# Optimization experiments

Measured on AMD Instinct MI355X. Metric: run time of the kernel, lower is better.

Reference implementation:

```python
import jax, jax.numpy as jnp
import numpy as np


def setup_inputs() -> dict:
    key = jax.random.key(0)
    k1, k2, k3 = jax.random.split(key, 3)
    N = 16384
    y = jax.random.normal(k1, (N,), dtype=jnp.float32)
    y_hat = jax.random.normal(k2, (N,), dtype=jnp.float32)
    status = jax.random.randint(k3, (N,), 0, 2, dtype=jnp.int32)
    return {"y": y, "y_hat": y_hat, "status": status}


def reference(y, y_hat, status):
    # Pairwise concordance index over all pairs i < j.
    # ge[i, j] = y[i] >= y[j]; le[i, j] = y[i] <= y[j]
    N = y.shape[0]
    ge = y[:, None] >= y[None, :]
    le = y[:, None] <= y[None, :]
    ge_hat = y_hat[:, None] >= y_hat[None, :]
    le_hat = y_hat[:, None] <= y_hat[None, :]
    st_i = (status == 1)[:, None]  # astatus_1 broadcast over j
    st_j = (status == 1)[None, :]  # bstatus_1 broadcast over i
    # upper-triangular mask (strict): pairs with j > i
    mask = jnp.triu(jnp.ones((N, N), dtype=bool), k=1)

    c1 = ge & ge_hat & st_j
    c2 = le & le_hat & st_i
    cc = (c1 | c2) & mask

    tp1 = le & st_i
    tp2 = ge & st_j
    tp = (tp1 | tp2) & mask

    c = jnp.sum(cc.astype(jnp.int32)).astype(jnp.float32)
    total_pairs = jnp.sum(tp.astype(jnp.int32)).astype(jnp.float32)
    return c / total_pairs
```

## Files before the change

kernel.cpp:

```cpp
#include <hip/hip_runtime.h>


#define BLOCK 256
#define TJ 256
#define IT 4
#define TI (BLOCK * IT)
#define GRID_PAIRS 1024


__global__ __launch_bounds__(256) void compact_kernel(
    const float* __restrict__ y, const float* __restrict__ yh,
    const int* __restrict__ status, int n,
    unsigned* __restrict__ cnts,
    float2* __restrict__ p1, float2* __restrict__ p0)
{
    int i = blockIdx.x * 256 + threadIdx.x;
    int lane = threadIdx.x & 63;
    bool act = i < n;
    float yv  = act ? y[i]  : 0.0f;
    float yhv = act ? yh[i] : 0.0f;
    bool st = act && (status[i] == 1);
    unsigned long long m1 = __ballot(st);
    unsigned long long m0 = __ballot(act && !st);
    unsigned long long lt = (1ull << lane) - 1ull;
    unsigned b1 = 0, b0 = 0;
    if (lane == 0) {
        b1 = atomicAdd(&cnts[0], (unsigned)__popcll(m1));
        b0 = atomicAdd(&cnts[1], (unsigned)__popcll(m0));
    }
    b1 = __shfl(b1, 0, 64);
    b0 = __shfl(b0, 0, 64);
    if (st) {
        p1[b1 + (unsigned)__popcll(m1 & lt)] = make_float2(yv, yhv);
    } else if (act) {
        p0[b0 + (unsigned)__popcll(m0 & lt)] = make_float2(yv, yhv);
    }
}

__global__ __launch_bounds__(BLOCK) void pairs_kernel(
    const unsigned* __restrict__ cnts,
    const float2* __restrict__ p1, const float2* __restrict__ p0,
    unsigned long long* __restrict__ acc, unsigned* __restrict__ done,
    float* __restrict__ out)
{
    __shared__ float2 s_j[TJ];
    const int tid = threadIdx.x;
    const unsigned K = cnts[0], M = cnts[1];
    const int ntJ  = (int)((K + TJ - 1) / TJ);
    const int ntIA = (int)((K + TI - 1) / TI);
    const int ntIB = (int)((M + TI - 1) / TI);
    const int ntA  = ntIA * ntJ;
    const int ntot = ntA + ntIB * ntJ;
    const float PINF = __int_as_float(0x7f800000);
    const float NINF = __int_as_float(0xff800000);

    unsigned accNE = 0, accBC = 0, accBG = 0;

    for (int t = blockIdx.x; t < ntot; t += gridDim.x) {
        bool isA = t < ntA;
        int tt = isA ? t : t - ntA;
        int ti = tt / ntJ;
        int tj = tt - ti * ntJ;

        {
            int jidx = tj * TJ + tid;
            float2 jv = p1[jidx];
            if ((unsigned)jidx >= K) jv = make_float2(PINF, NINF);
            s_j[tid] = jv;
        }
        __syncthreads();

        const float2* pi = isA ? p1 : p0;
        unsigned ilim = isA ? K : M;
        float2 v0, v1, v2, v3;
        {
            int ib = ti * TI + tid;
            float2 sA = make_float2(NINF, PINF);
            float2 sB = make_float2(NINF, NINF);
            float2 sent = isA ? sA : sB;
            v0 = pi[ib];              if ((unsigned)(ib)             >= ilim) v0 = sent;
            v1 = pi[ib + BLOCK];      if ((unsigned)(ib + BLOCK)     >= ilim) v1 = sent;
            v2 = pi[ib + 2 * BLOCK];  if ((unsigned)(ib + 2 * BLOCK) >= ilim) v2 = sent;
            v3 = pi[ib + 3 * BLOCK];  if ((unsigned)(ib + 3 * BLOCK) >= ilim) v3 = sent;
        }

        if (isA) {
            unsigned n0 = 0, n1 = 0;
#pragma unroll 8
            for (int jj = 0; jj < TJ; ++jj) {
                float2 p = s_j[jj];
                n0 += (unsigned)((v0.x >= p.x) != (v0.y >= p.y));
                n1 += (unsigned)((v1.x >= p.x) != (v1.y >= p.y));
                n0 += (unsigned)((v2.x >= p.x) != (v2.y >= p.y));
                n1 += (unsigned)((v3.x >= p.x) != (v3.y >= p.y));
            }
            accNE += n0 + n1;
        } else {
            unsigned g0 = 0, g1 = 0, c0 = 0, c1 = 0;
#pragma unroll 8
            for (int jj = 0; jj < TJ; ++jj) {
                float2 p = s_j[jj];
                bool a0 = v0.x >= p.x, b0 = v0.y >= p.y;
                bool a1 = v1.x >= p.x, b1 = v1.y >= p.y;
                bool a2 = v2.x >= p.x, b2 = v2.y >= p.y;
                bool a3 = v3.x >= p.x, b3 = v3.y >= p.y;
                g0 += (unsigned)a0; c0 += (unsigned)(a0 & b0);
                g1 += (unsigned)a1; c1 += (unsigned)(a1 & b1);
                g0 += (unsigned)a2; c0 += (unsigned)(a2 & b2);
                g1 += (unsigned)a3; c1 += (unsigned)(a3 & b3);
            }
            accBG += g0 + g1; accBC += c0 + c1;
        }
        __syncthreads();
    }

#pragma unroll
    for (int off = 32; off > 0; off >>= 1) {
        accNE += __shfl_down(accNE, off, 64);
        accBC += __shfl_down(accBC, off, 64);
        accBG += __shfl_down(accBG, off, 64);
    }
    __shared__ unsigned rN[4], rC[4], rG[4];
    int wav = tid >> 6, lane = tid & 63;
    if (lane == 0) { rN[wav] = accNE; rC[wav] = accBC; rG[wav] = accBG; }
    __syncthreads();
    if (tid == 0) {
        unsigned long long ne = (unsigned long long)rN[0] + rN[1] + rN[2] + rN[3];
        unsigned long long bc = (unsigned long long)rC[0] + rC[1] + rC[2] + rC[3];
        unsigned long long bg = (unsigned long long)rG[0] + rG[1] + rG[2] + rG[3];
        if (ne) atomicAdd(&acc[0], ne);
        if (bc) atomicAdd(&acc[1], bc);
        if (bg) atomicAdd(&acc[2], bg);
        __threadfence();
        if (atomicAdd(done, 1u) == (unsigned)(gridDim.x - 1)) {
            __threadfence();
            unsigned long long NE = atomicAdd(&acc[0], 0ull);
            unsigned long long BC = atomicAdd(&acc[1], 0ull);
            unsigned long long BG = atomicAdd(&acc[2], 0ull);
            unsigned long long Kl = K;
            unsigned long long slots = (unsigned long long)(ntIA * TI) *
                                       (unsigned long long)(ntJ * TJ);
            unsigned long long EQ = slots - NE;
            unsigned long long CC = EQ + 2ull * BC;
            unsigned long long TP = Kl * Kl + 2ull * BG;
            long long cn = (long long)CC - (long long)Kl;
            long long tn = (long long)TP - (long long)Kl;
            out[0] = (float)cn / (float)tn;
        }
    }
}

extern "C" void kernel_launch(void* const* d_in, const int* in_sizes, int n_in,
                              void* d_out, int out_size, void* d_ws, size_t ws_size,
                              hipStream_t stream) {
    const float* y      = (const float*)d_in[0];
    const float* y_hat  = (const float*)d_in[1];
    const int*   status = (const int*)d_in[2];
    float* out = (float*)d_out;
    int n = in_sizes[0];
    int stride = n + 1024;

    char* base = (char*)d_ws;
    unsigned* cnts = (unsigned*)base;
    unsigned long long* acc = (unsigned long long*)(base + 8);
    unsigned* done = (unsigned*)(base + 32);
    float2* p1 = (float2*)(base + 64);
    float2* p0 = p1 + stride;

    hipMemsetAsync(base, 0, 64, stream);

    hipLaunchKernelGGL(compact_kernel, dim3((n + 255) / 256), dim3(256), 0, stream,
                       y, y_hat, status, n, cnts, p1, p0);

    hipLaunchKernelGGL(pairs_kernel, dim3(GRID_PAIRS), dim3(BLOCK), 0, stream,
                       cnts, p1, p0, acc, done, out);
}
```

Measured before the change: 97.75 us.

## Use dynamic atomic tile scheduling with smaller i-tiles and NaN-select compare trick

Replaces the static grid-stride tile loop with a global atomic tile counter, so blocks pull work dynamically and load stays balanced. The i-tile is halved (2 items per thread instead of 4), which doubles the tile count and shared-memory loads per comparison but gives finer scheduling granularity. The concordant count now uses a select-to-NaN followed by one compare in place of an AND of two compares. This adds one atomic and one barrier per tile.

```diff
diff --git a/kernel.cpp b/kernel.cpp
--- a/kernel.cpp
+++ b/kernel.cpp
@@ -3,7 +3,7 @@
 
 #define BLOCK 256
 #define TJ 256
-#define IT 4
+#define IT 2
 #define TI (BLOCK * IT)
 #define GRID_PAIRS 1024
 
@@ -41,9 +41,10 @@
     const unsigned* __restrict__ cnts,
     const float2* __restrict__ p1, const float2* __restrict__ p0,
     unsigned long long* __restrict__ acc, unsigned* __restrict__ done,
-    float* __restrict__ out)
+    unsigned* __restrict__ tile_ctr, float* __restrict__ out)
 {
     __shared__ float2 s_j[TJ];
+    __shared__ int s_tile;
     const int tid = threadIdx.x;
     const unsigned K = cnts[0], M = cnts[1];
     const int ntJ  = (int)((K + TJ - 1) / TJ);
@@ -53,10 +54,16 @@
     const int ntot = ntA + ntIB * ntJ;
     const float PINF = __int_as_float(0x7f800000);
     const float NINF = __int_as_float(0xff800000);
+    const float NANF = __int_as_float(0x7fc00000);
 
-    unsigned accNE = 0, accBC = 0, accBG = 0;
+    unsigned aNE0 = 0, aNE1 = 0, aBG0 = 0, aBG1 = 0, aBC0 = 0, aBC1 = 0;
 
-    for (int t = blockIdx.x; t < ntot; t += gridDim.x) {
+    for (;;) {
+        if (tid == 0) s_tile = (int)atomicAdd(tile_ctr, 1u);
+        __syncthreads();
+        int t = s_tile;
+        if (t >= ntot) break;
+
         bool isA = t < ntA;
         int tt = isA ? t : t - ntA;
         int ti = tt / ntJ;
@@ -72,17 +79,12 @@
 
         const float2* pi = isA ? p1 : p0;
         unsigned ilim = isA ? K : M;
-        float2 v0, v1, v2, v3;
-        {
-            int ib = ti * TI + tid;
-            float2 sA = make_float2(NINF, PINF);
-            float2 sB = make_float2(NINF, NINF);
-            float2 sent = isA ? sA : sB;
-            v0 = pi[ib];              if ((unsigned)(ib)             >= ilim) v0 = sent;
-            v1 = pi[ib + BLOCK];      if ((unsigned)(ib + BLOCK)     >= ilim) v1 = sent;
-            v2 = pi[ib + 2 * BLOCK];  if ((unsigned)(ib + 2 * BLOCK) >= ilim) v2 = sent;
-            v3 = pi[ib + 3 * BLOCK];  if ((unsigned)(ib + 3 * BLOCK) >= ilim) v3 = sent;
-        }
+        int ib = ti * TI + tid;
+        float2 sA = make_float2(NINF, PINF);
+        float2 sB = make_float2(NINF, NINF);
+        float2 sent = isA ? sA : sB;
+        float2 v0 = pi[ib];          if ((unsigned)ib           >= ilim) v0 = sent;
+        float2 v1 = pi[ib + BLOCK];  if ((unsigned)(ib + BLOCK) >= ilim) v1 = sent;
 
         if (isA) {
             unsigned n0 = 0, n1 = 0;
@@ -91,28 +93,28 @@
                 float2 p = s_j[jj];
                 n0 += (unsigned)((v0.x >= p.x) != (v0.y >= p.y));
                 n1 += (unsigned)((v1.x >= p.x) != (v1.y >= p.y));
-                n0 += (unsigned)((v2.x >= p.x) != (v2.y >= p.y));
-                n1 += (unsigned)((v3.x >= p.x) != (v3.y >= p.y));
             }
-            accNE += n0 + n1;
+            aNE0 += n0; aNE1 += n1;
         } else {
             unsigned g0 = 0, g1 = 0, c0 = 0, c1 = 0;
 #pragma unroll 8
             for (int jj = 0; jj < TJ; ++jj) {
                 float2 p = s_j[jj];
-                bool a0 = v0.x >= p.x, b0 = v0.y >= p.y;
-                bool a1 = v1.x >= p.x, b1 = v1.y >= p.y;
-                bool a2 = v2.x >= p.x, b2 = v2.y >= p.y;
-                bool a3 = v3.x >= p.x, b3 = v3.y >= p.y;
-                g0 += (unsigned)a0; c0 += (unsigned)(a0 & b0);
-                g1 += (unsigned)a1; c1 += (unsigned)(a1 & b1);
-                g0 += (unsigned)a2; c0 += (unsigned)(a2 & b2);
-                g1 += (unsigned)a3; c1 += (unsigned)(a3 & b3);
+                g0 += (unsigned)(v0.x >= p.x);
+                float t0 = (v0.x >= p.x) ? v0.y : NANF;
+                c0 += (unsigned)(t0 >= p.y);
+                g1 += (unsigned)(v1.x >= p.x);
+                float t1 = (v1.x >= p.x) ? v1.y : NANF;
+                c1 += (unsigned)(t1 >= p.y);
             }
-            accBG += g0 + g1; accBC += c0 + c1;
+            aBG0 += g0; aBG1 += g1; aBC0 += c0; aBC1 += c1;
         }
         __syncthreads();
     }
+
+    unsigned accNE = aNE0 + aNE1;
+    unsigned accBG = aBG0 + aBG1;
+    unsigned accBC = aBC0 + aBC1;
 
 #pragma unroll
     for (int off = 32; off > 0; off >>= 1) {
@@ -164,6 +166,7 @@
     unsigned* cnts = (unsigned*)base;
     unsigned long long* acc = (unsigned long long*)(base + 8);
     unsigned* done = (unsigned*)(base + 32);
+    unsigned* tile_ctr = (unsigned*)(base + 36);
     float2* p1 = (float2*)(base + 64);
     float2* p0 = p1 + stride;
 
@@ -173,5 +176,5 @@
                        y, y_hat, status, n, cnts, p1, p0);
 
     hipLaunchKernelGGL(pairs_kernel, dim3(GRID_PAIRS), dim3(BLOCK), 0, stream,
-                       cnts, p1, p0, acc, done, out);
+                       cnts, p1, p0, acc, done, tile_ctr, out);
 }
```

Measured after the change: 127.1 us. 30.0% more time.
